# Kernel tuning notes

Measured on AMD Instinct MI355X. Metric: run time of the kernel, lower is better.

The kernel has to match this reference:

```python
import jax, jax.numpy as jnp
import numpy as np

NUM_HEAD = 12
DIM_MODEL = 768
HEAD_DIM = DIM_MODEL // NUM_HEAD


def setup_inputs() -> dict:
    key = jax.random.key(0)
    ks = jax.random.split(key, 4)
    B, S, D = 2, 2048, DIM_MODEL
    scale = 1.0 / np.sqrt(D)
    return {
        "v1": jax.random.normal(ks[0], (B, S, D), dtype=jnp.float32),
        "v1_mask": jnp.zeros((B, 1, 1, S), dtype=jnp.float32),
        "Wq": jax.random.normal(ks[1], (D, D), dtype=jnp.float32) * scale,
        "bq": jnp.zeros((D,), dtype=jnp.float32),
        "Wk": jax.random.normal(ks[2], (D, D), dtype=jnp.float32) * scale,
        "bk": jnp.zeros((D,), dtype=jnp.float32),
        "Wv": jax.random.normal(ks[3], (D, D), dtype=jnp.float32) * scale,
        "bv": jnp.zeros((D,), dtype=jnp.float32),
    }


def reference(v1, v1_mask, Wq, bq, Wk, bk, Wv, bv):
    B, S, D = v1.shape
    H, hd = NUM_HEAD, HEAD_DIM

    def split_heads(x):  # [B,S,D] -> [B,H,S,hd]
        return x.reshape(B, S, H, hd).transpose(0, 2, 1, 3)

    q = split_heads(v1 @ Wq + bq)
    k = split_heads(v1 @ Wk + bk)
    v = split_heads(v1 @ Wv + bv)

    scores = jnp.einsum("bhqd,bhkd->bhqk", q, k) / jnp.sqrt(jnp.float32(hd))
    scores = scores + v1_mask  # additive mask broadcasts over heads/query
    probs = jax.nn.softmax(scores, axis=-1)
    # dropout is identity in eval/reference mode
    ctx = jnp.einsum("bhqk,bhkd->bhqd", probs, v)
    return ctx.transpose(0, 2, 1, 3).reshape(B, S, D)
```

## Files before the change

### kernel.cpp

```cpp
#include <hip/hip_runtime.h>
#include <math.h>

#define B_SZ 2
#define S_SZ 2048
#define D_SZ 768
#define NH   12
#define HD   64
#define BH_T (B_SZ * NH)
#define M_TOT (B_SZ * S_SZ)

using bfrag = __attribute__((ext_vector_type(8))) short;
using ffrag = __attribute__((ext_vector_type(4))) float;

__device__ __forceinline__ unsigned short f2bf(float f) {
    unsigned int u = __float_as_uint(f);
    u += 0x7fffu + ((u >> 16) & 1u);
    return (unsigned short)(u >> 16);
}

__device__ __forceinline__ unsigned cvtpk(float lo, float hi) {
    unsigned r;
    asm("v_cvt_pk_bf16_f32 %0, %1, %2" : "=v"(r) : "v"(lo), "v"(hi));
    return r;
}

__device__ __forceinline__ float fexp2(float x) {
#if __has_builtin(__builtin_amdgcn_exp2f)
    return __builtin_amdgcn_exp2f(x);
#else
    float r;
    asm("v_exp_f32 %0, %1" : "=v"(r) : "v"(x));
    return r;
#endif
}

__device__ __forceinline__ void async16(void* lds, const void* gp) {
    __builtin_amdgcn_global_load_lds(
        (const __attribute__((address_space(1))) unsigned int*)gp,
        (__attribute__((address_space(3))) unsigned int*)lds,
        16, 0, 0);
}

__global__ __launch_bounds__(256) void prep(
    const float* __restrict__ v1,
    const float* __restrict__ Wq, const float* __restrict__ Wk,
    const float* __restrict__ Wv,
    unsigned short* __restrict__ v1b, unsigned short* __restrict__ Wt) {
    __shared__ float tile[64][65];
    const int bx = blockIdx.x;
    const int t = threadIdx.x;
    if (bx < 3072) {
        int i = (bx * 256 + t) * 4;
        float4 v = *(const float4*)&v1[i];
        ushort4 o;
        o.x = f2bf(v.x); o.y = f2bf(v.y); o.z = f2bf(v.z); o.w = f2bf(v.w);
        *(ushort4*)&v1b[i] = o;
    } else {
        int r = bx - 3072;
        int z = r / 144;
        int rr = r % 144;
        int n0 = (rr % 12) * 64, k0 = (rr / 12) * 64;
        const float* W = (z == 0) ? Wq : (z == 1) ? Wk : Wv;
        unsigned short* dst = Wt + (size_t)z * D_SZ * D_SZ;
        #pragma unroll
        for (int i = 0; i < 16; ++i) {
            int flat = i * 256 + t;
            int rr2 = flat >> 6, c = flat & 63;
            tile[rr2][c] = W[(size_t)(k0 + rr2) * D_SZ + n0 + c];
        }
        __syncthreads();
        #pragma unroll
        for (int i = 0; i < 16; ++i) {
            int flat = i * 256 + t;
            int rr2 = flat >> 6, c = flat & 63;
            dst[(size_t)(n0 + rr2) * D_SZ + k0 + c] = f2bf(tile[c][rr2]);
        }
    }
}

#define RP_LD 136

__global__ __launch_bounds__(256) void proj_gemm(
    const unsigned short* __restrict__ Ab,
    const unsigned short* __restrict__ Wt,
    const float* __restrict__ bq, const float* __restrict__ bk_,
    const float* __restrict__ bv_,
    unsigned short* __restrict__ Qb, unsigned short* __restrict__ Kb,
    unsigned short* __restrict__ Vtb) {
    const int z = blockIdx.z;
    const unsigned short* Bt = Wt + (size_t)z * D_SZ * D_SZ;
    const float* bias = (z == 0) ? bq : (z == 1) ? bk_ : bv_;

    __shared__ __attribute__((aligned(16)))
        unsigned short smem[2][128 * 64 + 128 * 64];
    const int t = threadIdx.x;
    const int lane = t & 63;
    const int w = t >> 6;
    const int wm = w & 1, wn = w >> 1;
    const int col = lane & 15;
    const int quad = lane >> 4;
    const int m0 = blockIdx.y * 128;
    const int n0 = blockIdx.x * 128;
    const int wbase = t & ~63;

    ffrag acc[4][4];
    #pragma unroll
    for (int i = 0; i < 4; ++i)
        #pragma unroll
        for (int j = 0; j < 4; ++j) { ffrag zf = {0.f, 0.f, 0.f, 0.f}; acc[i][j] = zf; }

    #pragma unroll
    for (int i = 0; i < 4; ++i) {
        int c = i * 256 + t;
        int row = c >> 3;
        int gcol = ((c & 7) ^ (row & 7)) * 8;
        async16(&smem[0][(size_t)(i * 256 + wbase) * 8],
                &Ab[(size_t)(m0 + row) * D_SZ + gcol]);
    }
    #pragma unroll
    for (int i = 0; i < 4; ++i) {
        int c = i * 256 + t;
        int row = c >> 3;
        int gcol = ((c & 7) ^ (row & 7)) * 8;
        async16(&smem[0][128 * 64 + (size_t)(i * 256 + wbase) * 8],
                &Bt[(size_t)(n0 + row) * D_SZ + gcol]);
    }

    const int nIter = D_SZ / 64;
    for (int it = 0; it < nIter; ++it) {
        const int cur = it & 1;
        __syncthreads();
        if (it + 1 < nIter) {
            const int kn = (it + 1) * 64;
            #pragma unroll
            for (int i = 0; i < 4; ++i) {
                int c = i * 256 + t;
                int row = c >> 3;
                int gcol = ((c & 7) ^ (row & 7)) * 8;
                async16(&smem[cur ^ 1][(size_t)(i * 256 + wbase) * 8],
                        &Ab[(size_t)(m0 + row) * D_SZ + kn + gcol]);
            }
            #pragma unroll
            for (int i = 0; i < 4; ++i) {
                int c = i * 256 + t;
                int row = c >> 3;
                int gcol = ((c & 7) ^ (row & 7)) * 8;
                async16(&smem[cur ^ 1][128 * 64 + (size_t)(i * 256 + wbase) * 8],
                        &Bt[(size_t)(n0 + row) * D_SZ + kn + gcol]);
            }
        }
        const unsigned short* As = &smem[cur][0];
        const unsigned short* Bs = &smem[cur][128 * 64];
        #pragma unroll
        for (int kk = 0; kk < 64; kk += 32) {
            const int cc = (kk >> 3) + quad;
            bfrag a[4], b[4];
            #pragma unroll
            for (int mi = 0; mi < 4; ++mi) {
                int row = wm * 64 + mi * 16 + col;
                a[mi] = *(const bfrag*)&As[row * 64 + ((cc ^ (row & 7)) * 8)];
            }
            #pragma unroll
            for (int ni = 0; ni < 4; ++ni) {
                int row = wn * 64 + ni * 16 + col;
                b[ni] = *(const bfrag*)&Bs[row * 64 + ((cc ^ (row & 7)) * 8)];
            }
            if (z == 2) {
                #pragma unroll
                for (int mi = 0; mi < 4; ++mi)
                    #pragma unroll
                    for (int ni = 0; ni < 4; ++ni)
                        acc[mi][ni] = __builtin_amdgcn_mfma_f32_16x16x32_bf16(
                            a[mi], b[ni], acc[mi][ni], 0, 0, 0);
            } else {
                #pragma unroll
                for (int mi = 0; mi < 4; ++mi)
                    #pragma unroll
                    for (int ni = 0; ni < 4; ++ni)
                        acc[mi][ni] = __builtin_amdgcn_mfma_f32_16x16x32_bf16(
                            b[ni], a[mi], acc[mi][ni], 0, 0, 0);
            }
        }
    }

    __syncthreads();
    unsigned short* rp = &smem[0][0];

    if (z < 2) {
        const float sc = (z == 0) ? 0.18033688f : 1.0f;
        #pragma unroll
        for (int mi = 0; mi < 4; ++mi) {
            int m_local = wm * 64 + mi * 16 + col;
            #pragma unroll
            for (int ni = 0; ni < 4; ++ni) {
                int n_base = wn * 64 + ni * 16 + quad * 4;
                float4 b4 = *(const float4*)&bias[n0 + n_base];
                uint2 pk;
                pk.x = (unsigned)f2bf((acc[mi][ni][0] + b4.x) * sc) |
                       ((unsigned)f2bf((acc[mi][ni][1] + b4.y) * sc) << 16);
                pk.y = (unsigned)f2bf((acc[mi][ni][2] + b4.z) * sc) |
                       ((unsigned)f2bf((acc[mi][ni][3] + b4.w) * sc) << 16);
                *(uint2*)&rp[m_local * RP_LD + n_base] = pk;
            }
        }
        __syncthreads();
        unsigned short* Out = (z == 0) ? Qb : Kb;
        #pragma unroll
        for (int j = 0; j < 8; ++j) {
            int flat = j * 256 + t;
            int row = flat >> 4;
            int ch = flat & 15;
            uint4 vv = *(const uint4*)&rp[row * RP_LD + ch * 8];
            int m = m0 + row;
            int bb = m >> 11, s = m & 2047;
            int h = (n0 >> 6) + (ch >> 3);
            int d = (ch & 7) * 8;
            *(uint4*)&Out[((size_t)(bb * NH + h) * S_SZ + s) * HD + d] = vv;
        }
    } else {
        #pragma unroll
        for (int ni = 0; ni < 4; ++ni) {
            int n_local = wn * 64 + ni * 16 + col;
            float bvv = bias[n0 + n_local];
            #pragma unroll
            for (int mi = 0; mi < 4; ++mi) {
                int m_base = wm * 64 + mi * 16 + quad * 4;
                uint2 pk;
                pk.x = (unsigned)f2bf(acc[mi][ni][0] + bvv) |
                       ((unsigned)f2bf(acc[mi][ni][1] + bvv) << 16);
                pk.y = (unsigned)f2bf(acc[mi][ni][2] + bvv) |
                       ((unsigned)f2bf(acc[mi][ni][3] + bvv) << 16);
                *(uint2*)&rp[n_local * RP_LD + m_base] = pk;
            }
        }
        __syncthreads();
        #pragma unroll
        for (int j = 0; j < 8; ++j) {
            int flat = j * 256 + t;
            int row = flat >> 4;
            int ch = flat & 15;
            uint4 vv = *(const uint4*)&rp[row * RP_LD + ch * 8];
            int n = n0 + row;
            int h = n >> 6, d = n & 63;
            int m = m0 + ch * 8;
            int bb = m >> 11, s = m & 2047;
            *(uint4*)&Vtb[((size_t)(bb * NH + h) * HD + d) * S_SZ + s] = vv;
        }
    }
}

__device__ __forceinline__ void attn_iter(
    int it, int cur,
    unsigned short (&Ks)[2][64 * 64], unsigned short (&Vs)[2][64 * 64],
    unsigned short* Pw,
    const unsigned short* Kg, const unsigned short* Vg, const float* mrow,
    const int (&srw)[2], const int (&sgc)[2], int wbase, int col, int quad,
    const bfrag (&aq)[2], float4 (&mc)[4], float4 (&mn)[4],
    ffrag (&o)[4], float& lsum) {
    const int nIter = S_SZ / 64;
    __syncthreads();
    if (it + 1 < nIter) {
        const int kn = (it + 1) * 64;
        #pragma unroll
        for (int i = 0; i < 2; ++i) {
            async16(&Ks[cur ^ 1][(size_t)(i * 256 + wbase) * 8],
                    &Kg[(size_t)(kn + srw[i]) * HD + sgc[i]]);
            async16(&Vs[cur ^ 1][(size_t)(i * 256 + wbase) * 8],
                    &Vg[(size_t)srw[i] * S_SZ + kn + sgc[i]]);
        }
        #pragma unroll
        for (int ni = 0; ni < 4; ++ni)
            mn[ni] = *(const float4*)&mrow[kn + ni * 16 + quad * 4];
    }

    ffrag s[4];
    __builtin_amdgcn_s_setprio(1);
    #pragma unroll
    for (int ni = 0; ni < 4; ++ni) {
        int brow = ni * 16 + col;
        bfrag bk0 = *(const bfrag*)&Ks[cur][brow * 64 + ((quad ^ (brow & 7)) * 8)];
        ffrag zf = {0.f, 0.f, 0.f, 0.f};
        s[ni] = __builtin_amdgcn_mfma_f32_16x16x32_bf16(bk0, aq[0], zf, 0, 0, 0);
    }
    #pragma unroll
    for (int ni = 0; ni < 4; ++ni) {
        int brow = ni * 16 + col;
        bfrag bk1 = *(const bfrag*)&Ks[cur][brow * 64 + (((4 + quad) ^ (brow & 7)) * 8)];
        s[ni] = __builtin_amdgcn_mfma_f32_16x16x32_bf16(bk1, aq[1], s[ni], 0, 0, 0);
    }
    __builtin_amdgcn_s_setprio(0);

    #pragma unroll
    for (int ni = 0; ni < 4; ++ni) {
        float4 m4 = mc[ni];
        float p0 = fexp2(fmaf(1.44269504f, m4.x, s[ni][0]));
        float p1 = fexp2(fmaf(1.44269504f, m4.y, s[ni][1]));
        float p2 = fexp2(fmaf(1.44269504f, m4.z, s[ni][2]));
        float p3 = fexp2(fmaf(1.44269504f, m4.w, s[ni][3]));
        lsum += ((p0 + p1) + (p2 + p3));
        uint2 pkv;
        pkv.x = cvtpk(p0, p1);
        pkv.y = cvtpk(p2, p3);
        int c = ni * 2 + (quad >> 1);
        *(uint2*)&Pw[col * 64 + ((c ^ (col & 7)) * 8) + (quad & 1) * 4] = pkv;
    }

    __builtin_amdgcn_s_setprio(1);
    #pragma unroll
    for (int kk = 0; kk < 2; ++kk) {
        const int cc = kk * 4 + quad;
        bfrag ap = *(const bfrag*)&Pw[col * 64 + ((cc ^ (col & 7)) * 8)];
        #pragma unroll
        for (int di = 0; di < 4; ++di) {
            int vrow = di * 16 + col;
            bfrag bv8 = *(const bfrag*)&Vs[cur][vrow * 64 + ((cc ^ (vrow & 7)) * 8)];
            o[di] = __builtin_amdgcn_mfma_f32_16x16x32_bf16(ap, bv8, o[di], 0, 0, 0);
        }
    }
    __builtin_amdgcn_s_setprio(0);
}

__global__ __launch_bounds__(256) void attn_mfma(
    const unsigned short* __restrict__ Qb, const unsigned short* __restrict__ Kb,
    const unsigned short* __restrict__ Vt, const float* __restrict__ mask,
    float* __restrict__ out) {
    __shared__ unsigned short Ks[2][64 * 64];
    __shared__ unsigned short Vs[2][64 * 64];
    __shared__ unsigned short Ps[4][16 * 64];

    const int t = threadIdx.x;
    const int lane = t & 63;
    const int w = t >> 6;
    const int col = lane & 15;
    const int quad = lane >> 4;
    const int q0 = blockIdx.x * 64;
    const int bh = blockIdx.y;
    const int b = bh / NH, h = bh % NH;
    const int wbase = t & ~63;

    const unsigned short* Qg = Qb + (size_t)bh * S_SZ * HD;
    const unsigned short* Kg = Kb + (size_t)bh * S_SZ * HD;
    const unsigned short* Vg = Vt + (size_t)bh * S_SZ * HD;
    const float* mrow = mask + (size_t)b * S_SZ;

    const int arow = w * 16 + col;
    bfrag aq[2];
    #pragma unroll
    for (int kk = 0; kk < 2; ++kk)
        aq[kk] = *(const bfrag*)&Qg[(size_t)(q0 + arow) * HD + (kk * 4 + quad) * 8];

    int srw[2], sgc[2];
    #pragma unroll
    for (int i = 0; i < 2; ++i) {
        int c = i * 256 + t;
        srw[i] = c >> 3;
        sgc[i] = ((c & 7) ^ (srw[i] & 7)) * 8;
    }

    #pragma unroll
    for (int i = 0; i < 2; ++i) {
        async16(&Ks[0][(size_t)(i * 256 + wbase) * 8],
                &Kg[(size_t)srw[i] * HD + sgc[i]]);
        async16(&Vs[0][(size_t)(i * 256 + wbase) * 8],
                &Vg[(size_t)srw[i] * S_SZ + sgc[i]]);
    }
    float4 mA[4], mB[4];
    #pragma unroll
    for (int ni = 0; ni < 4; ++ni)
        mA[ni] = *(const float4*)&mrow[ni * 16 + quad * 4];

    ffrag o[4];
    #pragma unroll
    for (int i = 0; i < 4; ++i) { ffrag zf = {0.f, 0.f, 0.f, 0.f}; o[i] = zf; }
    float lsum = 0.f;
    unsigned short* Pw = &Ps[w][0];

    for (int it2 = 0; it2 < (S_SZ / 64) / 2; ++it2) {
        attn_iter(it2 * 2 + 0, 0, Ks, Vs, Pw, Kg, Vg, mrow,
                  srw, sgc, wbase, col, quad, aq, mA, mB, o, lsum);
        attn_iter(it2 * 2 + 1, 1, Ks, Vs, Pw, Kg, Vg, mrow,
                  srw, sgc, wbase, col, quad, aq, mB, mA, o, lsum);
    }

    lsum += __shfl_xor(lsum, 16);
    lsum += __shfl_xor(lsum, 32);

    float inv[4];
    #pragma unroll
    for (int r = 0; r < 4; ++r)
        inv[r] = 1.0f / __shfl(lsum, quad * 4 + r);
    #pragma unroll
    for (int di = 0; di < 4; ++di) {
        int d = di * 16 + col;
        #pragma unroll
        for (int r = 0; r < 4; ++r) {
            int q = q0 + w * 16 + quad * 4 + r;
            out[((size_t)(b * S_SZ + q)) * D_SZ + h * HD + d] = o[di][r] * inv[r];
        }
    }
}

extern "C" void kernel_launch(void* const* d_in, const int* in_sizes, int n_in,
                              void* d_out, int out_size, void* d_ws, size_t ws_size,
                              hipStream_t stream) {
    const float* v1   = (const float*)d_in[0];
    const float* mask = (const float*)d_in[1];
    const float* Wq   = (const float*)d_in[2];
    const float* bq   = (const float*)d_in[3];
    const float* Wk   = (const float*)d_in[4];
    const float* bk   = (const float*)d_in[5];
    const float* Wv   = (const float*)d_in[6];
    const float* bv   = (const float*)d_in[7];
    float* out = (float*)d_out;

    char* ws = (char*)d_ws;
    const size_t per_b = (size_t)BH_T * S_SZ * HD * 2;
    unsigned short* Qb  = (unsigned short*)(ws);
    unsigned short* Kb  = (unsigned short*)(ws + per_b);
    unsigned short* Vtb = (unsigned short*)(ws + 2 * per_b);
    unsigned short* v1b = (unsigned short*)(ws + 3 * per_b);
    unsigned short* Wt  = (unsigned short*)(ws + 3 * per_b + (size_t)M_TOT * D_SZ * 2);

    prep<<<dim3(3072 + 432), 256, 0, stream>>>(v1, Wq, Wk, Wv, v1b, Wt);
    proj_gemm<<<dim3(6, 32, 3), 256, 0, stream>>>(v1b, Wt, bq, bk, bv, Qb, Kb, Vtb);
    attn_mfma<<<dim3(32, 24), 256, 0, stream>>>(Qb, Kb, Vtb, mask, out);
}
```

Before: 150.6 us.

## Process two query sub-tiles per wave in attention with 128-thread blocks

The attention kernel now runs 2 waves per block instead of 4, and each wave handles 32 query rows as two 16-row sub-tiles. Each K and V fragment read from LDS feeds two MFMAs, which halves LDS fragment reads per unit of compute. Cooperative K/V tile loading is redistributed over 128 threads. The cost is more registers per wave (two sets of accumulators, scores and P tiles), and fewer waves per block may reduce latency hiding and occupancy.

```diff
diff --git a/kernel.cpp b/kernel.cpp
--- a/kernel.cpp
+++ b/kernel.cpp
@@ -249,84 +249,100 @@
     }
 }
 
-__device__ __forceinline__ void attn_iter(
+__device__ __forceinline__ void attn_iter2(
     int it, int cur,
     unsigned short (&Ks)[2][64 * 64], unsigned short (&Vs)[2][64 * 64],
-    unsigned short* Pw,
+    unsigned short* Pw0, unsigned short* Pw1,
     const unsigned short* Kg, const unsigned short* Vg, const float* mrow,
-    const int (&srw)[2], const int (&sgc)[2], int wbase, int col, int quad,
-    const bfrag (&aq)[2], float4 (&mc)[4], float4 (&mn)[4],
-    ffrag (&o)[4], float& lsum) {
+    const int (&srw)[4], const int (&sgc)[4], int wbase, int col, int quad,
+    const bfrag (&aq)[2][2], float4 (&mc)[4], float4 (&mn)[4],
+    ffrag (&o0)[4], ffrag (&o1)[4], float& lsum0, float& lsum1) {
     const int nIter = S_SZ / 64;
     __syncthreads();
     if (it + 1 < nIter) {
         const int kn = (it + 1) * 64;
         #pragma unroll
-        for (int i = 0; i < 2; ++i) {
-            async16(&Ks[cur ^ 1][(size_t)(i * 256 + wbase) * 8],
+        for (int i = 0; i < 4; ++i)
+            async16(&Ks[cur ^ 1][(size_t)(i * 128 + wbase) * 8],
                     &Kg[(size_t)(kn + srw[i]) * HD + sgc[i]]);
-            async16(&Vs[cur ^ 1][(size_t)(i * 256 + wbase) * 8],
+        #pragma unroll
+        for (int i = 0; i < 4; ++i)
+            async16(&Vs[cur ^ 1][(size_t)(i * 128 + wbase) * 8],
                     &Vg[(size_t)srw[i] * S_SZ + kn + sgc[i]]);
-        }
         #pragma unroll
         for (int ni = 0; ni < 4; ++ni)
             mn[ni] = *(const float4*)&mrow[kn + ni * 16 + quad * 4];
     }
 
-    ffrag s[4];
+    ffrag s0[4], s1[4];
     __builtin_amdgcn_s_setprio(1);
     #pragma unroll
     for (int ni = 0; ni < 4; ++ni) {
         int brow = ni * 16 + col;
         bfrag bk0 = *(const bfrag*)&Ks[cur][brow * 64 + ((quad ^ (brow & 7)) * 8)];
         ffrag zf = {0.f, 0.f, 0.f, 0.f};
-        s[ni] = __builtin_amdgcn_mfma_f32_16x16x32_bf16(bk0, aq[0], zf, 0, 0, 0);
+        s0[ni] = __builtin_amdgcn_mfma_f32_16x16x32_bf16(bk0, aq[0][0], zf, 0, 0, 0);
+        s1[ni] = __builtin_amdgcn_mfma_f32_16x16x32_bf16(bk0, aq[1][0], zf, 0, 0, 0);
     }
     #pragma unroll
     for (int ni = 0; ni < 4; ++ni) {
         int brow = ni * 16 + col;
         bfrag bk1 = *(const bfrag*)&Ks[cur][brow * 64 + (((4 + quad) ^ (brow & 7)) * 8)];
-        s[ni] = __builtin_amdgcn_mfma_f32_16x16x32_bf16(bk1, aq[1], s[ni], 0, 0, 0);
+        s0[ni] = __builtin_amdgcn_mfma_f32_16x16x32_bf16(bk1, aq[0][1], s0[ni], 0, 0, 0);
+        s1[ni] = __builtin_amdgcn_mfma_f32_16x16x32_bf16(bk1, aq[1][1], s1[ni], 0, 0, 0);
     }
     __builtin_amdgcn_s_setprio(0);
 
     #pragma unroll
     for (int ni = 0; ni < 4; ++ni) {
         float4 m4 = mc[ni];
-        float p0 = fexp2(fmaf(1.44269504f, m4.x, s[ni][0]));
-        float p1 = fexp2(fmaf(1.44269504f, m4.y, s[ni][1]));
-        float p2 = fexp2(fmaf(1.44269504f, m4.z, s[ni][2]));
-        float p3 = fexp2(fmaf(1.44269504f, m4.w, s[ni][3]));
-        lsum += ((p0 + p1) + (p2 + p3));
-        uint2 pkv;
-        pkv.x = cvtpk(p0, p1);
-        pkv.y = cvtpk(p2, p3);
         int c = ni * 2 + (quad >> 1);
-        *(uint2*)&Pw[col * 64 + ((c ^ (col & 7)) * 8) + (quad & 1) * 4] = pkv;
+        int pa = col * 64 + ((c ^ (col & 7)) * 8) + (quad & 1) * 4;
+        {
+            float p0 = fexp2(fmaf(1.44269504f, m4.x, s0[ni][0]));
+            float p1 = fexp2(fmaf(1.44269504f, m4.y, s0[ni][1]));
+            float p2 = fexp2(fmaf(1.44269504f, m4.z, s0[ni][2]));
+            float p3 = fexp2(fmaf(1.44269504f, m4.w, s0[ni][3]));
+            lsum0 += ((p0 + p1) + (p2 + p3));
+            uint2 pkv; pkv.x = cvtpk(p0, p1); pkv.y = cvtpk(p2, p3);
+            *(uint2*)&Pw0[pa] = pkv;
+        }
+        {
+            float p0 = fexp2(fmaf(1.44269504f, m4.x, s1[ni][0]));
+            float p1 = fexp2(fmaf(1.44269504f, m4.y, s1[ni][1]));
+            float p2 = fexp2(fmaf(1.44269504f, m4.z, s1[ni][2]));
+            float p3 = fexp2(fmaf(1.44269504f, m4.w, s1[ni][3]));
+            lsum1 += ((p0 + p1) + (p2 + p3));
+            uint2 pkv; pkv.x = cvtpk(p0, p1); pkv.y = cvtpk(p2, p3);
+            *(uint2*)&Pw1[pa] = pkv;
+        }
     }
 
     __builtin_amdgcn_s_setprio(1);
     #pragma unroll
     for (int kk = 0; kk < 2; ++kk) {
         const int cc = kk * 4 + quad;
-        bfrag ap = *(const bfrag*)&Pw[col * 64 + ((cc ^ (col & 7)) * 8)];
+        int pra = col * 64 + ((cc ^ (col & 7)) * 8);
+        bfrag ap0 = *(const bfrag*)&Pw0[pra];
+        bfrag ap1 = *(const bfrag*)&Pw1[pra];
         #pragma unroll
         for (int di = 0; di < 4; ++di) {
             int vrow = di * 16 + col;
             bfrag bv8 = *(const bfrag*)&Vs[cur][vrow * 64 + ((cc ^ (vrow & 7)) * 8)];
-            o[di] = __builtin_amdgcn_mfma_f32_16x16x32_bf16(ap, bv8, o[di], 0, 0, 0);
+            o0[di] = __builtin_amdgcn_mfma_f32_16x16x32_bf16(ap0, bv8, o0[di], 0, 0, 0);
+            o1[di] = __builtin_amdgcn_mfma_f32_16x16x32_bf16(ap1, bv8, o1[di], 0, 0, 0);
         }
     }
     __builtin_amdgcn_s_setprio(0);
 }
 
-__global__ __launch_bounds__(256) void attn_mfma(
+__global__ __launch_bounds__(128) void attn_mfma(
     const unsigned short* __restrict__ Qb, const unsigned short* __restrict__ Kb,
     const unsigned short* __restrict__ Vt, const float* __restrict__ mask,
     float* __restrict__ out) {
     __shared__ unsigned short Ks[2][64 * 64];
     __shared__ unsigned short Vs[2][64 * 64];
-    __shared__ unsigned short Ps[4][16 * 64];
+    __shared__ unsigned short Ps[2][2][16 * 64];
 
     const int t = threadIdx.x;
     const int lane = t & 63;
@@ -343,25 +359,28 @@
     const unsigned short* Vg = Vt + (size_t)bh * S_SZ * HD;
     const float* mrow = mask + (size_t)b * S_SZ;
 
-    const int arow = w * 16 + col;
-    bfrag aq[2];
-    #pragma unroll
-    for (int kk = 0; kk < 2; ++kk)
-        aq[kk] = *(const bfrag*)&Qg[(size_t)(q0 + arow) * HD + (kk * 4 + quad) * 8];
-
-    int srw[2], sgc[2];
-    #pragma unroll
-    for (int i = 0; i < 2; ++i) {
-        int c = i * 256 + t;
+    bfrag aq[2][2];
+    #pragma unroll
+    for (int qs = 0; qs < 2; ++qs) {
+        int arow = w * 32 + qs * 16 + col;
+        #pragma unroll
+        for (int kk = 0; kk < 2; ++kk)
+            aq[qs][kk] = *(const bfrag*)&Qg[(size_t)(q0 + arow) * HD + (kk * 4 + quad) * 8];
+    }
+
+    int srw[4], sgc[4];
+    #pragma unroll
+    for (int i = 0; i < 4; ++i) {
+        int c = i * 128 + t;
         srw[i] = c >> 3;
         sgc[i] = ((c & 7) ^ (srw[i] & 7)) * 8;
     }
 
     #pragma unroll
-    for (int i = 0; i < 2; ++i) {
-        async16(&Ks[0][(size_t)(i * 256 + wbase) * 8],
+    for (int i = 0; i < 4; ++i) {
+        async16(&Ks[0][(size_t)(i * 128 + wbase) * 8],
                 &Kg[(size_t)srw[i] * HD + sgc[i]]);
-        async16(&Vs[0][(size_t)(i * 256 + wbase) * 8],
+        async16(&Vs[0][(size_t)(i * 128 + wbase) * 8],
                 &Vg[(size_t)srw[i] * S_SZ + sgc[i]]);
     }
     float4 mA[4], mB[4];
@@ -369,33 +388,42 @@
     for (int ni = 0; ni < 4; ++ni)
         mA[ni] = *(const float4*)&mrow[ni * 16 + quad * 4];
 
-    ffrag o[4];
-    #pragma unroll
-    for (int i = 0; i < 4; ++i) { ffrag zf = {0.f, 0.f, 0.f, 0.f}; o[i] = zf; }
-    float lsum = 0.f;
-    unsigned short* Pw = &Ps[w][0];
+    ffrag o0[4], o1[4];
+    #pragma unroll
+    for (int i = 0; i < 4; ++i) {
+        ffrag zf = {0.f, 0.f, 0.f, 0.f};
+        o0[i] = zf; o1[i] = zf;
+    }
+    float lsum0 = 0.f, lsum1 = 0.f;
+    unsigned short* Pw0 = &Ps[w][0][0];
+    unsigned short* Pw1 = &Ps[w][1][0];
 
     for (int it2 = 0; it2 < (S_SZ / 64) / 2; ++it2) {
-        attn_iter(it2 * 2 + 0, 0, Ks, Vs, Pw, Kg, Vg, mrow,
-                  srw, sgc, wbase, col, quad, aq, mA, mB, o, lsum);
-        attn_iter(it2 * 2 + 1, 1, Ks, Vs, Pw, Kg, Vg, mrow,
-                  srw, sgc, wbase, col, quad, aq, mB, mA, o, lsum);
-    }
-
-    lsum += __shfl_xor(lsum, 16);
-    lsum += __shfl_xor(lsum, 32);
-
-    float inv[4];
-    #pragma unroll
-    for (int r = 0; r < 4; ++r)
-        inv[r] = 1.0f / __shfl(lsum, quad * 4 + r);
+        attn_iter2(it2 * 2 + 0, 0, Ks, Vs, Pw0, Pw1, Kg, Vg, mrow,
+                   srw, sgc, wbase, col, quad, aq, mA, mB, o0, o1, lsum0, lsum1);
+        attn_iter2(it2 * 2 + 1, 1, Ks, Vs, Pw0, Pw1, Kg, Vg, mrow,
+                   srw, sgc, wbase, col, quad, aq, mB, mA, o0, o1, lsum0, lsum1);
+    }
+
+    lsum0 += __shfl_xor(lsum0, 16);
+    lsum0 += __shfl_xor(lsum0, 32);
+    lsum1 += __shfl_xor(lsum1, 16);
+    lsum1 += __shfl_xor(lsum1, 32);
+
+    float inv0[4], inv1[4];
+    #pragma unroll
+    for (int r = 0; r < 4; ++r) {
+        inv0[r] = 1.0f / __shfl(lsum0, quad * 4 + r);
+        inv1[r] = 1.0f / __shfl(lsum1, quad * 4 + r);
+    }
     #pragma unroll
     for (int di = 0; di < 4; ++di) {
         int d = di * 16 + col;
         #pragma unroll
         for (int r = 0; r < 4; ++r) {
-            int q = q0 + w * 16 + quad * 4 + r;
-            out[((size_t)(b * S_SZ + q)) * D_SZ + h * HD + d] = o[di][r] * inv[r];
+            int qa = q0 + w * 32 + quad * 4 + r;
+            out[((size_t)(b * S_SZ + qa)) * D_SZ + h * HD + d] = o0[di][r] * inv0[r];
+            out[((size_t)(b * S_SZ + qa + 16)) * D_SZ + h * HD + d] = o1[di][r] * inv1[r];
         }
     }
 }
@@ -423,5 +451,5 @@
 
     prep<<<dim3(3072 + 432), 256, 0, stream>>>(v1, Wq, Wk, Wv, v1b, Wt);
     proj_gemm<<<dim3(6, 32, 3), 256, 0, stream>>>(v1b, Wt, bq, bk, bv, Qb, Kb, Vtb);
-    attn_mfma<<<dim3(32, 24), 256, 0, stream>>>(Qb, Kb, Vtb, mask, out);
-}
+    attn_mfma<<<dim3(32, 24), 128, 0, stream>>>(Qb, Kb, Vtb, mask, out);
+}
```

Result: slower. 188.0 us (+24.8%).
